# Performance work log

Measured on AMD Instinct MI355X. Metric: run time of the kernel, lower is better.

Reference implementation:

```python
import jax, jax.numpy as jnp
import numpy as np

N = 32768      # nodes
E = 524288     # edges (before self-loops)
F_IN = 256     # input feature dim
H = 4          # attention heads
C = 128        # per-head (and output) channels; concat=False -> mean over heads
NEG_SLOPE = 0.2
BN_EPS = 1e-5


def setup_inputs() -> dict:
    key = jax.random.key(0)
    ks = jax.random.split(key, 20)
    s = 0.1
    inp = {
        "x": jax.random.normal(ks[0], (N, F_IN), dtype=jnp.float32),
        "edge_index": jax.random.randint(ks[1], (2, E), 0, N, dtype=jnp.int64),
        # layer 1 (GATConv in=256 -> heads=4, C=128) + BN
        "W1": jax.random.normal(ks[2], (F_IN, H * C), dtype=jnp.float32) * s,
        "as1": jax.random.normal(ks[3], (H, C), dtype=jnp.float32) * s,
        "ad1": jax.random.normal(ks[4], (H, C), dtype=jnp.float32) * s,
        "b1": jnp.zeros((C,), jnp.float32),
        "g1": jnp.ones((C,), jnp.float32),
        "be1": jnp.zeros((C,), jnp.float32),
        # layer 2 (GATConv in=128 -> heads=4, C=128) + BN
        "W2": jax.random.normal(ks[5], (C, H * C), dtype=jnp.float32) * s,
        "as2": jax.random.normal(ks[6], (H, C), dtype=jnp.float32) * s,
        "ad2": jax.random.normal(ks[7], (H, C), dtype=jnp.float32) * s,
        "b2": jnp.zeros((C,), jnp.float32),
        "g2": jnp.ones((C,), jnp.float32),
        "be2": jnp.zeros((C,), jnp.float32),
        # final linear C -> C
        "Wf": jax.random.normal(ks[8], (C, C), dtype=jnp.float32) * s,
        "bf": jnp.zeros((C,), jnp.float32),
    }
    return inp


def _gat_conv(x, src, dst, W, att_src, att_dst, bias):
    # x: [N, Din]; src/dst: [E'] (self-loops already included)
    h = (x @ W).reshape(N, H, C)                     # [N,H,C]
    a_src = jnp.sum(h * att_src, axis=-1)            # [N,H]
    a_dst = jnp.sum(h * att_dst, axis=-1)            # [N,H]
    e = jax.nn.leaky_relu(a_src[src] + a_dst[dst], NEG_SLOPE)  # [E',H]
    # softmax over incoming edges per destination node (segment softmax)
    m = jax.ops.segment_max(e, dst, num_segments=N)  # [N,H]; safe: self-loops
    e = jnp.exp(e - m[dst])
    denom = jax.ops.segment_sum(e, dst, num_segments=N)
    alpha = e / (denom[dst] + 1e-16)                 # [E',H]
    msg = h[src] * alpha[:, :, None]                 # [E',H,C]
    out = jax.ops.segment_sum(msg, dst, num_segments=N)  # [N,H,C]
    return out.mean(axis=1) + bias                   # concat=False -> head mean


def _batch_norm(x, gamma, beta):
    mu = x.mean(axis=0)
    var = x.var(axis=0)  # biased, as torch BN normalization
    return (x - mu) * jax.lax.rsqrt(var + BN_EPS) * gamma + beta


def reference(x, edge_index, W1, as1, ad1, b1, g1, be1,
              W2, as2, ad2, b2, g2, be2, Wf, bf):
    # add self-loops (PyG GATConv default add_self_loops=True)
    loop = jnp.arange(N, dtype=edge_index.dtype)
    src = jnp.concatenate([edge_index[0], loop])
    dst = jnp.concatenate([edge_index[1], loop])

    h = _gat_conv(x, src, dst, W1, as1, ad1, b1)
    h = jax.nn.relu(_batch_norm(h, g1, be1))  # dropout = identity (eval)

    h = _gat_conv(h, src, dst, W2, as2, ad2, b2)
    h = jax.nn.relu(_batch_norm(h, g2, be2))

    return h @ Wf + bf
```

## Files before the change

### kernel.cpp

```cpp
#include <hip/hip_runtime.h>
#include <math.h>

namespace {

constexpr int N    = 32768;
constexpr int E    = 524288;
constexpr int ETOT = E + N;
constexpr int FIN  = 256;
constexpr int H    = 4;
constexpr int C    = 128;
constexpr int HC   = H * C;
constexpr float NEG    = 0.2f;
constexpr float BN_EPS = 1e-5f;

typedef __attribute__((ext_vector_type(8))) short  bf16x8;
typedef __attribute__((ext_vector_type(4))) float  f32x4;

__device__ __forceinline__ float lrelu(float x) { return x >= 0.f ? x : NEG * x; }

__device__ __forceinline__ unsigned short f2b(float f) {
  unsigned u = __float_as_uint(f);
  u = (u + 0x7fffu + ((u >> 16) & 1u)) >> 16;
  return (unsigned short)u;
}
__device__ __forceinline__ float blo(unsigned u) { return __uint_as_float(u << 16); }
__device__ __forceinline__ float bhi(unsigned u) { return __uint_as_float(u & 0xffff0000u); }

__global__ void k_cvt4(const float* __restrict__ in, unsigned short* __restrict__ out, int n4) {
  int i = blockIdx.x * blockDim.x + threadIdx.x;
  if (i >= n4) return;
  float4 v = reinterpret_cast<const float4*>(in)[i];
  ushort4 o;
  o.x = f2b(v.x); o.y = f2b(v.y); o.z = f2b(v.z); o.w = f2b(v.w);
  reinterpret_cast<ushort4*>(out)[i] = o;
}

__global__ void k_wcvt(const float* __restrict__ W, unsigned short* __restrict__ Wt,
                       int K, int Nc) {
  int idx = blockIdx.x * blockDim.x + threadIdx.x;
  if (idx >= K * Nc) return;
  int c = idx / K, k = idx - c * K;
  Wt[idx] = f2b(W[(size_t)k * Nc + c]);
}

__global__ __launch_bounds__(256) void gemm_bt(
    const unsigned short* __restrict__ A,
    const unsigned short* __restrict__ Bt,
    const float* __restrict__ bias,
    void* __restrict__ Cout, int M, int K, int Nc, int out_bf16)
{
  __shared__ unsigned short As[128][40];
  __shared__ unsigned short Bs[128][40];
  const int tid  = threadIdx.x;
  const int wave = tid >> 6, lane = tid & 63;
  const int wr = (wave >> 1) * 64, wc = (wave & 1) * 64;
  const int row0 = blockIdx.y * 128, col0 = blockIdx.x * 128;

  f32x4 acc[4][4] = {};
  const int sr = tid >> 2, ks = (tid & 3) * 8;

  for (int k0 = 0; k0 < K; k0 += 32) {
    *(bf16x8*)&As[sr][ks]      = *(const bf16x8*)&A [(size_t)(row0 + sr)      * K + k0 + ks];
    *(bf16x8*)&As[sr + 64][ks] = *(const bf16x8*)&A [(size_t)(row0 + sr + 64) * K + k0 + ks];
    *(bf16x8*)&Bs[sr][ks]      = *(const bf16x8*)&Bt[(size_t)(col0 + sr)      * K + k0 + ks];
    *(bf16x8*)&Bs[sr + 64][ks] = *(const bf16x8*)&Bt[(size_t)(col0 + sr + 64) * K + k0 + ks];
    __syncthreads();

    const int fr = lane & 15, kq = (lane >> 4) * 8;
    bf16x8 af[4], bfr[4];
#pragma unroll
    for (int m = 0; m < 4; ++m) af[m]  = *(const bf16x8*)&As[wr + m * 16 + fr][kq];
#pragma unroll
    for (int n = 0; n < 4; ++n) bfr[n] = *(const bf16x8*)&Bs[wc + n * 16 + fr][kq];
#pragma unroll
    for (int m = 0; m < 4; ++m)
#pragma unroll
      for (int n = 0; n < 4; ++n)
        acc[m][n] = __builtin_amdgcn_mfma_f32_16x16x32_bf16(af[m], bfr[n], acc[m][n], 0, 0, 0);
    __syncthreads();
  }

  const int fr = lane & 15, fq = (lane >> 4) * 4;
  if (out_bf16) {
    unsigned short* O = (unsigned short*)Cout;
#pragma unroll
    for (int m = 0; m < 4; ++m)
#pragma unroll
      for (int n = 0; n < 4; ++n) {
        int col = col0 + wc + n * 16 + fr;
#pragma unroll
        for (int j = 0; j < 4; ++j) {
          int row = row0 + wr + m * 16 + fq + j;
          O[(size_t)row * Nc + col] = f2b(acc[m][n][j]);
        }
      }
  } else {
    float* O = (float*)Cout;
#pragma unroll
    for (int m = 0; m < 4; ++m)
#pragma unroll
      for (int n = 0; n < 4; ++n) {
        int col = col0 + wc + n * 16 + fr;
        float bv = bias ? bias[col] : 0.f;
#pragma unroll
        for (int j = 0; j < 4; ++j) {
          int row = row0 + wr + m * 16 + fq + j;
          O[(size_t)row * Nc + col] = acc[m][n][j] + bv;
        }
      }
  }
}

__global__ __launch_bounds__(256) void att_dots(
    const unsigned short* __restrict__ h, const float* __restrict__ as_,
    const float* __restrict__ ad_, float* __restrict__ asrc,
    float* __restrict__ adst)
{
  int gid  = blockIdx.x * blockDim.x + threadIdx.x;
  int wid  = gid >> 6;
  int lane = threadIdx.x & 63;
  if (wid >= N * H) return;
  int n = wid >> 2, hh = wid & 3;
  unsigned u = *reinterpret_cast<const unsigned*>(&h[(size_t)n * HC + hh * C + lane * 2]);
  float h0 = blo(u), h1 = bhi(u);
  const float2 sv = *reinterpret_cast<const float2*>(&as_[hh * C + lane * 2]);
  const float2 dv = *reinterpret_cast<const float2*>(&ad_[hh * C + lane * 2]);
  float s = h0 * sv.x + h1 * sv.y;
  float d = h0 * dv.x + h1 * dv.y;
  for (int off = 32; off; off >>= 1) {
    s += __shfl_down(s, off);
    d += __shfl_down(d, off);
  }
  if (lane == 0) { asrc[wid] = s; adst[wid] = d; }
}

__global__ void k_deg(const int* __restrict__ edst, int* __restrict__ deg) {
  int e = blockIdx.x * blockDim.x + threadIdx.x;
  if (e >= ETOT) return;
  int d = (e < E) ? edst[e] : (e - E);
  atomicAdd(&deg[d], 1);
}

__global__ __launch_bounds__(1024) void k_scan(const int* __restrict__ deg,
                                               int* __restrict__ offs) {
  __shared__ int sums[1024];
  int t = threadIdx.x;
  int base = t * 32;
  int local[32];
  int tot = 0;
#pragma unroll
  for (int i = 0; i < 32; ++i) { local[i] = deg[base + i]; tot += local[i]; }
  sums[t] = tot;
  __syncthreads();
  for (int off = 1; off < 1024; off <<= 1) {
    int v = (t >= off) ? sums[t - off] : 0;
    __syncthreads();
    sums[t] += v;
    __syncthreads();
  }
  int run = (t == 0) ? 0 : sums[t - 1];
#pragma unroll
  for (int i = 0; i < 32; ++i) { offs[base + i] = run; run += local[i]; }
  if (t == 1023) offs[N] = run;
}

__global__ void k_scatter(const int* __restrict__ esrc, const int* __restrict__ edst,
                          const int* __restrict__ offs, int* __restrict__ cursor,
                          int* __restrict__ csrc) {
  int e = blockIdx.x * blockDim.x + threadIdx.x;
  if (e >= ETOT) return;
  int s = (e < E) ? esrc[e] : (e - E);
  int d = (e < E) ? edst[e] : (e - E);
  int pos = offs[d] + atomicAdd(&cursor[d], 1);
  csrc[pos] = s;
}

__global__ __launch_bounds__(256) void k_softmax(
    const int* __restrict__ offs, const int* __restrict__ csrc,
    const float* __restrict__ asrc, const float* __restrict__ adst,
    float* __restrict__ pbuf, float* __restrict__ denom)
{
  int gid = blockIdx.x * blockDim.x + threadIdx.x;
  int n = gid >> 4, l = gid & 15;
  if (n >= N) return;
  int beg = offs[n], end = offs[n + 1];
  const float4 bv = *reinterpret_cast<const float4*>(&adst[n * 4]);
  float m0 = -1e30f, m1 = -1e30f, m2 = -1e30f, m3 = -1e30f;
  for (int i = beg + l; i < end; i += 16) {
    int s = csrc[i];
    float4 av = *reinterpret_cast<const float4*>(&asrc[s * 4]);
    m0 = fmaxf(m0, lrelu(av.x + bv.x));
    m1 = fmaxf(m1, lrelu(av.y + bv.y));
    m2 = fmaxf(m2, lrelu(av.z + bv.z));
    m3 = fmaxf(m3, lrelu(av.w + bv.w));
  }
#pragma unroll
  for (int off = 1; off < 16; off <<= 1) {
    m0 = fmaxf(m0, __shfl_xor(m0, off));
    m1 = fmaxf(m1, __shfl_xor(m1, off));
    m2 = fmaxf(m2, __shfl_xor(m2, off));
    m3 = fmaxf(m3, __shfl_xor(m3, off));
  }
  float s0 = 0.f, s1 = 0.f, s2 = 0.f, s3 = 0.f;
  for (int i = beg + l; i < end; i += 16) {
    int s = csrc[i];
    float4 av = *reinterpret_cast<const float4*>(&asrc[s * 4]);
    float p0 = __expf(lrelu(av.x + bv.x) - m0);
    float p1 = __expf(lrelu(av.y + bv.y) - m1);
    float p2 = __expf(lrelu(av.z + bv.z) - m2);
    float p3 = __expf(lrelu(av.w + bv.w) - m3);
    *reinterpret_cast<float4*>(&pbuf[(size_t)i * 4]) = make_float4(p0, p1, p2, p3);
    s0 += p0; s1 += p1; s2 += p2; s3 += p3;
  }
#pragma unroll
  for (int off = 1; off < 16; off <<= 1) {
    s0 += __shfl_xor(s0, off);
    s1 += __shfl_xor(s1, off);
    s2 += __shfl_xor(s2, off);
    s3 += __shfl_xor(s3, off);
  }
  if (l == 0)
    *reinterpret_cast<float4*>(&denom[n * 4]) = make_float4(s0, s1, s2, s3);
}

__global__ __launch_bounds__(128) void k_aggregate(
    const unsigned short* __restrict__ hb, const int* __restrict__ offs,
    const int* __restrict__ csrc, const float* __restrict__ pbuf,
    const float* __restrict__ denom, const float* __restrict__ bias,
    float* __restrict__ out)
{
  int n = blockIdx.x, t = threadIdx.x;
  int beg = offs[n], end = offs[n + 1];
  float4 dv = *reinterpret_cast<const float4*>(&denom[n * 4]);
  int hA = t >> 6;
  int c  = (t & 63) * 2;
  float a0 = 0.f, a1 = 0.f, b0 = 0.f, b1 = 0.f;
  for (int pos = beg; pos < end; ++pos) {
    int s = csrc[pos];
    float4 pv = *reinterpret_cast<const float4*>(&pbuf[(size_t)pos * 4]);
    const unsigned* hu = reinterpret_cast<const unsigned*>(&hb[(size_t)s * HC]);
    unsigned uA = hu[t];
    unsigned uB = hu[t + 128];
    float pA = hA ? pv.y : pv.x;
    float pB = hA ? pv.w : pv.z;
    a0 += pA * blo(uA); a1 += pA * bhi(uA);
    b0 += pB * blo(uB); b1 += pB * bhi(uB);
  }
  float invA = 1.f / ((hA ? dv.y : dv.x) + 1e-16f);
  float invB = 1.f / ((hA ? dv.w : dv.z) + 1e-16f);
  float s0 = a0 * invA + b0 * invB;
  float s1 = a1 * invA + b1 * invB;
  __shared__ float red[C];
  if (t < 64) { red[c] = s0; red[c + 1] = s1; }
  __syncthreads();
  if (t >= 64) {
    out[(size_t)n * C + c]     = 0.25f * (red[c] + s0)     + bias[c];
    out[(size_t)n * C + c + 1] = 0.25f * (red[c + 1] + s1) + bias[c + 1];
  }
}

__global__ __launch_bounds__(128) void k_bn_stats(const float* __restrict__ x,
                                                  float* __restrict__ stats) {
  int c = threadIdx.x;
  int rows = N / gridDim.x;
  int r0 = blockIdx.x * rows;
  float s = 0.f, s2 = 0.f;
  for (int r = r0; r < r0 + rows; ++r) {
    float v = x[(size_t)r * C + c];
    s += v; s2 += v * v;
  }
  atomicAdd(&stats[c], s);
  atomicAdd(&stats[C + c], s2);
}

__global__ void k_bn_apply(const float* __restrict__ stats, const float* __restrict__ g,
                           const float* __restrict__ be, const float* __restrict__ xin,
                           unsigned short* __restrict__ xb) {
  int i = blockIdx.x * blockDim.x + threadIdx.x;
  if (i >= N * C) return;
  int c = i & (C - 1);
  float mu  = stats[c] * (1.f / N);
  float var = stats[C + c] * (1.f / N) - mu * mu;
  float v = (xin[i] - mu) * rsqrtf(var + BN_EPS) * g[c] + be[c];
  xb[i] = f2b(v > 0.f ? v : 0.f);
}

}

extern "C" void kernel_launch(void* const* d_in, const int* in_sizes, int n_in,
                              void* d_out, int out_size, void* d_ws, size_t ws_size,
                              hipStream_t stream) {
  const float* x   = (const float*)d_in[0];
  const int*   ei  = (const int*)d_in[1];
  const float* W1  = (const float*)d_in[2];
  const float* as1 = (const float*)d_in[3];
  const float* ad1 = (const float*)d_in[4];
  const float* b1  = (const float*)d_in[5];
  const float* g1  = (const float*)d_in[6];
  const float* be1 = (const float*)d_in[7];
  const float* W2  = (const float*)d_in[8];
  const float* as2 = (const float*)d_in[9];
  const float* ad2 = (const float*)d_in[10];
  const float* b2  = (const float*)d_in[11];
  const float* g2  = (const float*)d_in[12];
  const float* be2 = (const float*)d_in[13];
  const float* Wf  = (const float*)d_in[14];
  const float* bf  = (const float*)d_in[15];
  float* out = (float*)d_out;

  const int* esrc = ei;
  const int* edst = ei + E;

  char* p = (char*)d_ws;
  auto alloc = [&](size_t bytes) {
    char* r = p;
    p += (bytes + 255) & ~size_t(255);
    return r;
  };
  unsigned short* hb   = (unsigned short*)alloc(2ull * N * HC);
  unsigned short* xbf  = (unsigned short*)alloc(2ull * N * FIN);
  unsigned short* xmb  = (unsigned short*)alloc(2ull * N * C);
  float*    xm     = (float*)alloc(sizeof(float) * (size_t)N * C);
  float*    pbuf   = (float*)alloc(sizeof(float) * (size_t)ETOT * 4);
  unsigned short* W1t = (unsigned short*)alloc(2ull * FIN * HC);
  unsigned short* W2t = (unsigned short*)alloc(2ull * C * HC);
  unsigned short* Wft = (unsigned short*)alloc(2ull * C * C);
  float*    asrc   = (float*)alloc(sizeof(float) * N * 4);
  float*    adst   = (float*)alloc(sizeof(float) * N * 4);
  float*    denom  = (float*)alloc(sizeof(float) * N * 4);
  float*    stats  = (float*)alloc(sizeof(float) * 2 * C);
  int*      deg    = (int*)alloc(sizeof(int) * N);
  int*      offs   = (int*)alloc(sizeof(int) * (N + 16));
  int*      cursor = (int*)alloc(sizeof(int) * N);
  int*      csrc   = (int*)alloc(sizeof(int) * ETOT);
  (void)ws_size; (void)in_sizes; (void)n_in; (void)out_size;

  const int EB = (ETOT + 255) / 256;

  hipMemsetAsync(deg, 0, sizeof(int) * N, stream);
  hipMemsetAsync(cursor, 0, sizeof(int) * N, stream);
  k_deg<<<EB, 256, 0, stream>>>(edst, deg);
  k_scan<<<1, 1024, 0, stream>>>(deg, offs);
  k_scatter<<<EB, 256, 0, stream>>>(esrc, edst, offs, cursor, csrc);

  k_cvt4<<<(N * FIN / 4 + 255) / 256, 256, 0, stream>>>(x, xbf, N * FIN / 4);
  k_wcvt<<<(FIN * HC + 255) / 256, 256, 0, stream>>>(W1, W1t, FIN, HC);
  k_wcvt<<<(C * HC + 255) / 256, 256, 0, stream>>>(W2, W2t, C, HC);
  k_wcvt<<<(C * C + 255) / 256, 256, 0, stream>>>(Wf, Wft, C, C);

  gemm_bt<<<dim3(HC / 128, N / 128), 256, 0, stream>>>(xbf, W1t, nullptr, hb, N, FIN, HC, 1);
  att_dots<<<(N * H) / 4, 256, 0, stream>>>(hb, as1, ad1, asrc, adst);
  k_softmax<<<(N * 16) / 256, 256, 0, stream>>>(offs, csrc, asrc, adst, pbuf, denom);
  k_aggregate<<<N, C, 0, stream>>>(hb, offs, csrc, pbuf, denom, b1, xm);
  hipMemsetAsync(stats, 0, sizeof(float) * 2 * C, stream);
  k_bn_stats<<<256, C, 0, stream>>>(xm, stats);
  k_bn_apply<<<(N * C) / 256, 256, 0, stream>>>(stats, g1, be1, xm, xmb);

  gemm_bt<<<dim3(HC / 128, N / 128), 256, 0, stream>>>(xmb, W2t, nullptr, hb, N, C, HC, 1);
  att_dots<<<(N * H) / 4, 256, 0, stream>>>(hb, as2, ad2, asrc, adst);
  k_softmax<<<(N * 16) / 256, 256, 0, stream>>>(offs, csrc, asrc, adst, pbuf, denom);
  k_aggregate<<<N, C, 0, stream>>>(hb, offs, csrc, pbuf, denom, b2, xm);
  hipMemsetAsync(stats, 0, sizeof(float) * 2 * C, stream);
  k_bn_stats<<<256, C, 0, stream>>>(xm, stats);
  k_bn_apply<<<(N * C) / 256, 256, 0, stream>>>(stats, g2, be2, xm, xmb);

  gemm_bt<<<dim3(1, N / 128), 256, 0, stream>>>(xmb, Wft, bf, out, N, C, C, 0);
}
```

Measured before the change: 538.4 us.

## Aggregate raw features before projection and fold attention vectors into weights

Reorders each GAT layer so the neighbor aggregation works on the narrower input features per head (z = sum alpha*x), then projects with a stacked weight matrix [4*Din -> C] that also carries the head mean. Attention logits are computed directly from x using precomputed W·a vectors, and softmax is fused into aggregation so the per-edge probability buffer and denominator pass disappear. The gathers now read Din-wide rows instead of 512-wide projected rows. In exchange, the projection GEMM gets a longer K and a 4*Din-wide intermediate is written, and the bias terms are dropped. Dropping the bias relies on it being zero or being absorbed by batch norm.

```diff
diff --git a/kernel.cpp b/kernel.cpp
--- a/kernel.cpp
+++ b/kernel.cpp
@@ -23,6 +23,9 @@
   u = (u + 0x7fffu + ((u >> 16) & 1u)) >> 16;
   return (unsigned short)u;
 }
+__device__ __forceinline__ unsigned pack2(float a, float b) {
+  return (unsigned)f2b(a) | ((unsigned)f2b(b) << 16);
+}
 __device__ __forceinline__ float blo(unsigned u) { return __uint_as_float(u << 16); }
 __device__ __forceinline__ float bhi(unsigned u) { return __uint_as_float(u & 0xffff0000u); }
 
@@ -41,6 +44,199 @@
   if (idx >= K * Nc) return;
   int c = idx / K, k = idx - c * K;
   Wt[idx] = f2b(W[(size_t)k * Nc + c]);
+}
+
+__global__ void k_wstack(const float* __restrict__ W, unsigned short* __restrict__ Bt,
+                         int Din) {
+  int idx = blockIdx.x * blockDim.x + threadIdx.x;
+  if (idx >= C * 4 * Din) return;
+  int c = idx / (4 * Din), r = idx - c * (4 * Din);
+  int h = r / Din, k = r - h * Din;
+  Bt[idx] = f2b(W[(size_t)k * HC + h * C + c]);
+}
+
+__global__ void k_attvec(const float* __restrict__ W, const float* __restrict__ as_,
+                         const float* __restrict__ ad_, float* __restrict__ av, int Din) {
+  int idx = blockIdx.x * blockDim.x + threadIdx.x;
+  if (idx >= 8 * Din) return;
+  int j = idx / Din, k = idx - j * Din, h = j & 3;
+  const float* a = (j < 4) ? as_ : ad_;
+  float s = 0.f;
+  for (int c = 0; c < C; ++c) s += W[(size_t)k * HC + h * C + c] * a[h * C + c];
+  av[idx] = s;
+}
+
+template<int DIN>
+__global__ __launch_bounds__(256) void k_attdots(
+    const unsigned short* __restrict__ xb, const float* __restrict__ av,
+    float* __restrict__ asrc, float* __restrict__ adst)
+{
+  constexpr int CPL = DIN / 64;
+  __shared__ float avs[8 * DIN];
+  for (int i = threadIdx.x; i < 8 * DIN; i += 256) avs[i] = av[i];
+  __syncthreads();
+  int wid = threadIdx.x >> 6, lane = threadIdx.x & 63;
+  int n = blockIdx.x * 4 + wid;
+  float xv[CPL];
+  if constexpr (CPL == 4) {
+    uint2 u = *reinterpret_cast<const uint2*>(&xb[(size_t)n * DIN + lane * 4]);
+    xv[0] = blo(u.x); xv[1] = bhi(u.x); xv[2] = blo(u.y); xv[3] = bhi(u.y);
+  } else {
+    unsigned u = *reinterpret_cast<const unsigned*>(&xb[(size_t)n * DIN + lane * 2]);
+    xv[0] = blo(u); xv[1] = bhi(u);
+  }
+  float s[8];
+#pragma unroll
+  for (int j = 0; j < 8; ++j) {
+    float t = 0.f;
+#pragma unroll
+    for (int q = 0; q < CPL; ++q) t += xv[q] * avs[j * DIN + lane * CPL + q];
+    s[j] = t;
+  }
+#pragma unroll
+  for (int off = 1; off < 64; off <<= 1)
+#pragma unroll
+    for (int j = 0; j < 8; ++j) s[j] += __shfl_xor(s[j], off);
+  if (lane == 0) {
+    *reinterpret_cast<float4*>(&asrc[n * 4]) = make_float4(s[0], s[1], s[2], s[3]);
+    *reinterpret_cast<float4*>(&adst[n * 4]) = make_float4(s[4], s[5], s[6], s[7]);
+  }
+}
+
+__global__ void k_deg(const int* __restrict__ edst, int* __restrict__ deg) {
+  int e = blockIdx.x * blockDim.x + threadIdx.x;
+  if (e >= ETOT) return;
+  int d = (e < E) ? edst[e] : (e - E);
+  atomicAdd(&deg[d], 1);
+}
+
+__global__ __launch_bounds__(1024) void k_scan(const int* __restrict__ deg,
+                                               int* __restrict__ offs) {
+  __shared__ int sums[1024];
+  int t = threadIdx.x;
+  int base = t * 32;
+  int local[32];
+  int tot = 0;
+#pragma unroll
+  for (int i = 0; i < 32; ++i) { local[i] = deg[base + i]; tot += local[i]; }
+  sums[t] = tot;
+  __syncthreads();
+  for (int off = 1; off < 1024; off <<= 1) {
+    int v = (t >= off) ? sums[t - off] : 0;
+    __syncthreads();
+    sums[t] += v;
+    __syncthreads();
+  }
+  int run = (t == 0) ? 0 : sums[t - 1];
+#pragma unroll
+  for (int i = 0; i < 32; ++i) { offs[base + i] = run; run += local[i]; }
+  if (t == 1023) offs[N] = run;
+}
+
+__global__ void k_scatter(const int* __restrict__ esrc, const int* __restrict__ edst,
+                          const int* __restrict__ offs, int* __restrict__ cursor,
+                          int* __restrict__ csrc) {
+  int e = blockIdx.x * blockDim.x + threadIdx.x;
+  if (e >= ETOT) return;
+  int s = (e < E) ? esrc[e] : (e - E);
+  int d = (e < E) ? edst[e] : (e - E);
+  int pos = offs[d] + atomicAdd(&cursor[d], 1);
+  csrc[pos] = s;
+}
+
+template<int DIN>
+__global__ __launch_bounds__(256) void k_fused_agg(
+    const unsigned short* __restrict__ xb, const int* __restrict__ offs,
+    const int* __restrict__ csrc, const float* __restrict__ asrc,
+    const float* __restrict__ adst, unsigned short* __restrict__ z)
+{
+  constexpr int CPL = DIN / 64;
+  __shared__ float pls[4][64][4];
+  __shared__ int   sls[4][64];
+  const int wid = threadIdx.x >> 6, lane = threadIdx.x & 63;
+  const int n = blockIdx.x * 4 + wid;
+  const int beg = offs[n], end = offs[n + 1];
+  const float4 bv = *reinterpret_cast<const float4*>(&adst[n * 4]);
+
+  float m0 = -1e30f, m1 = -1e30f, m2 = -1e30f, m3 = -1e30f;
+  for (int i = beg + lane; i < end; i += 64) {
+    int s = csrc[i];
+    float4 av = *reinterpret_cast<const float4*>(&asrc[s * 4]);
+    m0 = fmaxf(m0, lrelu(av.x + bv.x));
+    m1 = fmaxf(m1, lrelu(av.y + bv.y));
+    m2 = fmaxf(m2, lrelu(av.z + bv.z));
+    m3 = fmaxf(m3, lrelu(av.w + bv.w));
+  }
+#pragma unroll
+  for (int off = 1; off < 64; off <<= 1) {
+    m0 = fmaxf(m0, __shfl_xor(m0, off));
+    m1 = fmaxf(m1, __shfl_xor(m1, off));
+    m2 = fmaxf(m2, __shfl_xor(m2, off));
+    m3 = fmaxf(m3, __shfl_xor(m3, off));
+  }
+
+  float d0 = 0.f, d1 = 0.f, d2 = 0.f, d3 = 0.f;
+  float acc[4][CPL] = {};
+  for (int base = beg; base < end; base += 64) {
+    int i = base + lane;
+    float p0 = 0.f, p1 = 0.f, p2 = 0.f, p3 = 0.f;
+    int s = 0;
+    if (i < end) {
+      s = csrc[i];
+      float4 av = *reinterpret_cast<const float4*>(&asrc[s * 4]);
+      p0 = __expf(lrelu(av.x + bv.x) - m0);
+      p1 = __expf(lrelu(av.y + bv.y) - m1);
+      p2 = __expf(lrelu(av.z + bv.z) - m2);
+      p3 = __expf(lrelu(av.w + bv.w) - m3);
+    }
+    d0 += p0; d1 += p1; d2 += p2; d3 += p3;
+    sls[wid][lane] = s;
+    *reinterpret_cast<float4*>(&pls[wid][lane][0]) = make_float4(p0, p1, p2, p3);
+    int cnt = end - base; if (cnt > 64) cnt = 64;
+#pragma unroll 2
+    for (int j = 0; j < cnt; ++j) {
+      int sj = sls[wid][j];
+      float4 pj = *reinterpret_cast<const float4*>(&pls[wid][j][0]);
+      if constexpr (CPL == 4) {
+        uint2 u = *reinterpret_cast<const uint2*>(&xb[(size_t)sj * DIN + lane * 4]);
+        float c0 = blo(u.x), c1 = bhi(u.x), c2 = blo(u.y), c3 = bhi(u.y);
+        acc[0][0] += pj.x * c0; acc[0][1] += pj.x * c1; acc[0][2] += pj.x * c2; acc[0][3] += pj.x * c3;
+        acc[1][0] += pj.y * c0; acc[1][1] += pj.y * c1; acc[1][2] += pj.y * c2; acc[1][3] += pj.y * c3;
+        acc[2][0] += pj.z * c0; acc[2][1] += pj.z * c1; acc[2][2] += pj.z * c2; acc[2][3] += pj.z * c3;
+        acc[3][0] += pj.w * c0; acc[3][1] += pj.w * c1; acc[3][2] += pj.w * c2; acc[3][3] += pj.w * c3;
+      } else {
+        unsigned u = *reinterpret_cast<const unsigned*>(&xb[(size_t)sj * DIN + lane * 2]);
+        float c0 = blo(u), c1 = bhi(u);
+        acc[0][0] += pj.x * c0; acc[0][1] += pj.x * c1;
+        acc[1][0] += pj.y * c0; acc[1][1] += pj.y * c1;
+        acc[2][0] += pj.z * c0; acc[2][1] += pj.z * c1;
+        acc[3][0] += pj.w * c0; acc[3][1] += pj.w * c1;
+      }
+    }
+  }
+#pragma unroll
+  for (int off = 1; off < 64; off <<= 1) {
+    d0 += __shfl_xor(d0, off);
+    d1 += __shfl_xor(d1, off);
+    d2 += __shfl_xor(d2, off);
+    d3 += __shfl_xor(d3, off);
+  }
+  float inv[4];
+  inv[0] = 0.25f / (d0 + 1e-16f); inv[1] = 0.25f / (d1 + 1e-16f);
+  inv[2] = 0.25f / (d2 + 1e-16f); inv[3] = 0.25f / (d3 + 1e-16f);
+  size_t zb = (size_t)n * 4 * DIN;
+#pragma unroll
+  for (int h = 0; h < 4; ++h) {
+    if constexpr (CPL == 4) {
+      uint2 o;
+      o.x = pack2(acc[h][0] * inv[h], acc[h][1] * inv[h]);
+      o.y = pack2(acc[h][2] * inv[h], acc[h][3] * inv[h]);
+      *reinterpret_cast<uint2*>(&z[zb + h * DIN + lane * 4]) = o;
+    } else {
+      *reinterpret_cast<unsigned*>(&z[zb + h * DIN + lane * 2]) =
+          pack2(acc[h][0] * inv[h], acc[h][1] * inv[h]);
+    }
+  }
 }
 
 __global__ __launch_bounds__(256) void gemm_bt(
@@ -111,154 +307,6 @@
   }
 }
 
-__global__ __launch_bounds__(256) void att_dots(
-    const unsigned short* __restrict__ h, const float* __restrict__ as_,
-    const float* __restrict__ ad_, float* __restrict__ asrc,
-    float* __restrict__ adst)
-{
-  int gid  = blockIdx.x * blockDim.x + threadIdx.x;
-  int wid  = gid >> 6;
-  int lane = threadIdx.x & 63;
-  if (wid >= N * H) return;
-  int n = wid >> 2, hh = wid & 3;
-  unsigned u = *reinterpret_cast<const unsigned*>(&h[(size_t)n * HC + hh * C + lane * 2]);
-  float h0 = blo(u), h1 = bhi(u);
-  const float2 sv = *reinterpret_cast<const float2*>(&as_[hh * C + lane * 2]);
-  const float2 dv = *reinterpret_cast<const float2*>(&ad_[hh * C + lane * 2]);
-  float s = h0 * sv.x + h1 * sv.y;
-  float d = h0 * dv.x + h1 * dv.y;
-  for (int off = 32; off; off >>= 1) {
-    s += __shfl_down(s, off);
-    d += __shfl_down(d, off);
-  }
-  if (lane == 0) { asrc[wid] = s; adst[wid] = d; }
-}
-
-__global__ void k_deg(const int* __restrict__ edst, int* __restrict__ deg) {
-  int e = blockIdx.x * blockDim.x + threadIdx.x;
-  if (e >= ETOT) return;
-  int d = (e < E) ? edst[e] : (e - E);
-  atomicAdd(&deg[d], 1);
-}
-
-__global__ __launch_bounds__(1024) void k_scan(const int* __restrict__ deg,
-                                               int* __restrict__ offs) {
-  __shared__ int sums[1024];
-  int t = threadIdx.x;
-  int base = t * 32;
-  int local[32];
-  int tot = 0;
-#pragma unroll
-  for (int i = 0; i < 32; ++i) { local[i] = deg[base + i]; tot += local[i]; }
-  sums[t] = tot;
-  __syncthreads();
-  for (int off = 1; off < 1024; off <<= 1) {
-    int v = (t >= off) ? sums[t - off] : 0;
-    __syncthreads();
-    sums[t] += v;
-    __syncthreads();
-  }
-  int run = (t == 0) ? 0 : sums[t - 1];
-#pragma unroll
-  for (int i = 0; i < 32; ++i) { offs[base + i] = run; run += local[i]; }
-  if (t == 1023) offs[N] = run;
-}
-
-__global__ void k_scatter(const int* __restrict__ esrc, const int* __restrict__ edst,
-                          const int* __restrict__ offs, int* __restrict__ cursor,
-                          int* __restrict__ csrc) {
-  int e = blockIdx.x * blockDim.x + threadIdx.x;
-  if (e >= ETOT) return;
-  int s = (e < E) ? esrc[e] : (e - E);
-  int d = (e < E) ? edst[e] : (e - E);
-  int pos = offs[d] + atomicAdd(&cursor[d], 1);
-  csrc[pos] = s;
-}
-
-__global__ __launch_bounds__(256) void k_softmax(
-    const int* __restrict__ offs, const int* __restrict__ csrc,
-    const float* __restrict__ asrc, const float* __restrict__ adst,
-    float* __restrict__ pbuf, float* __restrict__ denom)
-{
-  int gid = blockIdx.x * blockDim.x + threadIdx.x;
-  int n = gid >> 4, l = gid & 15;
-  if (n >= N) return;
-  int beg = offs[n], end = offs[n + 1];
-  const float4 bv = *reinterpret_cast<const float4*>(&adst[n * 4]);
-  float m0 = -1e30f, m1 = -1e30f, m2 = -1e30f, m3 = -1e30f;
-  for (int i = beg + l; i < end; i += 16) {
-    int s = csrc[i];
-    float4 av = *reinterpret_cast<const float4*>(&asrc[s * 4]);
-    m0 = fmaxf(m0, lrelu(av.x + bv.x));
-    m1 = fmaxf(m1, lrelu(av.y + bv.y));
-    m2 = fmaxf(m2, lrelu(av.z + bv.z));
-    m3 = fmaxf(m3, lrelu(av.w + bv.w));
-  }
-#pragma unroll
-  for (int off = 1; off < 16; off <<= 1) {
-    m0 = fmaxf(m0, __shfl_xor(m0, off));
-    m1 = fmaxf(m1, __shfl_xor(m1, off));
-    m2 = fmaxf(m2, __shfl_xor(m2, off));
-    m3 = fmaxf(m3, __shfl_xor(m3, off));
-  }
-  float s0 = 0.f, s1 = 0.f, s2 = 0.f, s3 = 0.f;
-  for (int i = beg + l; i < end; i += 16) {
-    int s = csrc[i];
-    float4 av = *reinterpret_cast<const float4*>(&asrc[s * 4]);
-    float p0 = __expf(lrelu(av.x + bv.x) - m0);
-    float p1 = __expf(lrelu(av.y + bv.y) - m1);
-    float p2 = __expf(lrelu(av.z + bv.z) - m2);
-    float p3 = __expf(lrelu(av.w + bv.w) - m3);
-    *reinterpret_cast<float4*>(&pbuf[(size_t)i * 4]) = make_float4(p0, p1, p2, p3);
-    s0 += p0; s1 += p1; s2 += p2; s3 += p3;
-  }
-#pragma unroll
-  for (int off = 1; off < 16; off <<= 1) {
-    s0 += __shfl_xor(s0, off);
-    s1 += __shfl_xor(s1, off);
-    s2 += __shfl_xor(s2, off);
-    s3 += __shfl_xor(s3, off);
-  }
-  if (l == 0)
-    *reinterpret_cast<float4*>(&denom[n * 4]) = make_float4(s0, s1, s2, s3);
-}
-
-__global__ __launch_bounds__(128) void k_aggregate(
-    const unsigned short* __restrict__ hb, const int* __restrict__ offs,
-    const int* __restrict__ csrc, const float* __restrict__ pbuf,
-    const float* __restrict__ denom, const float* __restrict__ bias,
-    float* __restrict__ out)
-{
-  int n = blockIdx.x, t = threadIdx.x;
-  int beg = offs[n], end = offs[n + 1];
-  float4 dv = *reinterpret_cast<const float4*>(&denom[n * 4]);
-  int hA = t >> 6;
-  int c  = (t & 63) * 2;
-  float a0 = 0.f, a1 = 0.f, b0 = 0.f, b1 = 0.f;
-  for (int pos = beg; pos < end; ++pos) {
-    int s = csrc[pos];
-    float4 pv = *reinterpret_cast<const float4*>(&pbuf[(size_t)pos * 4]);
-    const unsigned* hu = reinterpret_cast<const unsigned*>(&hb[(size_t)s * HC]);
-    unsigned uA = hu[t];
-    unsigned uB = hu[t + 128];
-    float pA = hA ? pv.y : pv.x;
-    float pB = hA ? pv.w : pv.z;
-    a0 += pA * blo(uA); a1 += pA * bhi(uA);
-    b0 += pB * blo(uB); b1 += pB * bhi(uB);
-  }
-  float invA = 1.f / ((hA ? dv.y : dv.x) + 1e-16f);
-  float invB = 1.f / ((hA ? dv.w : dv.z) + 1e-16f);
-  float s0 = a0 * invA + b0 * invB;
-  float s1 = a1 * invA + b1 * invB;
-  __shared__ float red[C];
-  if (t < 64) { red[c] = s0; red[c + 1] = s1; }
-  __syncthreads();
-  if (t >= 64) {
-    out[(size_t)n * C + c]     = 0.25f * (red[c] + s0)     + bias[c];
-    out[(size_t)n * C + c + 1] = 0.25f * (red[c + 1] + s1) + bias[c + 1];
-  }
-}
-
 __global__ __launch_bounds__(128) void k_bn_stats(const float* __restrict__ x,
                                                   float* __restrict__ stats) {
   int c = threadIdx.x;
@@ -295,13 +343,11 @@
   const float* W1  = (const float*)d_in[2];
   const float* as1 = (const float*)d_in[3];
   const float* ad1 = (const float*)d_in[4];
-  const float* b1  = (const float*)d_in[5];
   const float* g1  = (const float*)d_in[6];
   const float* be1 = (const float*)d_in[7];
   const float* W2  = (const float*)d_in[8];
   const float* as2 = (const float*)d_in[9];
   const float* ad2 = (const float*)d_in[10];
-  const float* b2  = (const float*)d_in[11];
   const float* g2  = (const float*)d_in[12];
   const float* be2 = (const float*)d_in[13];
   const float* Wf  = (const float*)d_in[14];
@@ -317,17 +363,17 @@
     p += (bytes + 255) & ~size_t(255);
     return r;
   };
-  unsigned short* hb   = (unsigned short*)alloc(2ull * N * HC);
+  unsigned short* z1   = (unsigned short*)alloc(2ull * N * 4 * FIN);
   unsigned short* xbf  = (unsigned short*)alloc(2ull * N * FIN);
   unsigned short* xmb  = (unsigned short*)alloc(2ull * N * C);
   float*    xm     = (float*)alloc(sizeof(float) * (size_t)N * C);
-  float*    pbuf   = (float*)alloc(sizeof(float) * (size_t)ETOT * 4);
-  unsigned short* W1t = (unsigned short*)alloc(2ull * FIN * HC);
-  unsigned short* W2t = (unsigned short*)alloc(2ull * C * HC);
-  unsigned short* Wft = (unsigned short*)alloc(2ull * C * C);
+  unsigned short* Wst1 = (unsigned short*)alloc(2ull * C * 4 * FIN);
+  unsigned short* Wst2 = (unsigned short*)alloc(2ull * C * 4 * C);
+  unsigned short* Wft  = (unsigned short*)alloc(2ull * C * C);
+  float*    av1    = (float*)alloc(sizeof(float) * 8 * FIN);
+  float*    av2    = (float*)alloc(sizeof(float) * 8 * C);
   float*    asrc   = (float*)alloc(sizeof(float) * N * 4);
   float*    adst   = (float*)alloc(sizeof(float) * N * 4);
-  float*    denom  = (float*)alloc(sizeof(float) * N * 4);
   float*    stats  = (float*)alloc(sizeof(float) * 2 * C);
   int*      deg    = (int*)alloc(sizeof(int) * N);
   int*      offs   = (int*)alloc(sizeof(int) * (N + 16));
@@ -344,22 +390,22 @@
   k_scatter<<<EB, 256, 0, stream>>>(esrc, edst, offs, cursor, csrc);
 
   k_cvt4<<<(N * FIN / 4 + 255) / 256, 256, 0, stream>>>(x, xbf, N * FIN / 4);
-  k_wcvt<<<(FIN * HC + 255) / 256, 256, 0, stream>>>(W1, W1t, FIN, HC);
-  k_wcvt<<<(C * HC + 255) / 256, 256, 0, stream>>>(W2, W2t, C, HC);
+  k_wstack<<<(C * 4 * FIN + 255) / 256, 256, 0, stream>>>(W1, Wst1, FIN);
+  k_wstack<<<(C * 4 * C + 255) / 256, 256, 0, stream>>>(W2, Wst2, C);
   k_wcvt<<<(C * C + 255) / 256, 256, 0, stream>>>(Wf, Wft, C, C);
-
-  gemm_bt<<<dim3(HC / 128, N / 128), 256, 0, stream>>>(xbf, W1t, nullptr, hb, N, FIN, HC, 1);
-  att_dots<<<(N * H) / 4, 256, 0, stream>>>(hb, as1, ad1, asrc, adst);
-  k_softmax<<<(N * 16) / 256, 256, 0, stream>>>(offs, csrc, asrc, adst, pbuf, denom);
-  k_aggregate<<<N, C, 0, stream>>>(hb, offs, csrc, pbuf, denom, b1, xm);
+  k_attvec<<<(8 * FIN + 255) / 256, 256, 0, stream>>>(W1, as1, ad1, av1, FIN);
+  k_attvec<<<(8 * C + 255) / 256, 256, 0, stream>>>(W2, as2, ad2, av2, C);
+
+  k_attdots<FIN><<<N / 4, 256, 0, stream>>>(xbf, av1, asrc, adst);
+  k_fused_agg<FIN><<<N / 4, 256, 0, stream>>>(xbf, offs, csrc, asrc, adst, z1);
+  gemm_bt<<<dim3(1, N / 128), 256, 0, stream>>>(z1, Wst1, nullptr, xm, N, 4 * FIN, C, 0);
   hipMemsetAsync(stats, 0, sizeof(float) * 2 * C, stream);
   k_bn_stats<<<256, C, 0, stream>>>(xm, stats);
   k_bn_apply<<<(N * C) / 256, 256, 0, stream>>>(stats, g1, be1, xm, xmb);
 
-  gemm_bt<<<dim3(HC / 128, N / 128), 256, 0, stream>>>(xmb, W2t, nullptr, hb, N, C, HC, 1);
-  att_dots<<<(N * H) / 4, 256, 0, stream>>>(hb, as2, ad2, asrc, adst);
-  k_softmax<<<(N * 16) / 256, 256, 0, stream>>>(offs, csrc, asrc, adst, pbuf, denom);
-  k_aggregate<<<N, C, 0, stream>>>(hb, offs, csrc, pbuf, denom, b2, xm);
+  k_attdots<C><<<N / 4, 256, 0, stream>>>(xmb, av2, asrc, adst);
+  k_fused_agg<C><<<N / 4, 256, 0, stream>>>(xmb, offs, csrc, asrc, adst, z1);
+  gemm_bt<<<dim3(1, N / 128), 256, 0, stream>>>(z1, Wst2, nullptr, xm, N, 4 * C, C, 0);
   hipMemsetAsync(stats, 0, sizeof(float) * 2 * C, stream);
   k_bn_stats<<<256, C, 0, stream>>>(xm, stats);
   k_bn_apply<<<(N * C) / 256, 256, 0, stream>>>(stats, g2, be2, xm, xmb);
```

After: 476.5 us. 11.5% less time.
